# Performance work log

Hardware: AMD Instinct MI355X
Metric: run time of the kernel (lower is better)

## Reference

```python
import jax, jax.numpy as jnp
import numpy as np

NUM_CLUSTERS = 16
CHANNELS = 256
UPDATE_RATE = 0.2
# channels % num_clusters == 0 -> all cluster capacities equal
_BASE = CHANNELS // NUM_CLUSTERS
_REM = CHANNELS % NUM_CLUSTERS
CLUSTER_SIZES = jnp.asarray([_BASE + 1] * _REM + [_BASE] * (NUM_CLUSTERS - _REM), dtype=jnp.int32)


def _cdist(a, b):
    # euclidean pairwise distance, batched over leading dims
    d2 = (jnp.sum(a * a, -1)[..., :, None]
          + jnp.sum(b * b, -1)[..., None, :]
          - 2.0 * (a @ jnp.swapaxes(b, -1, -2)))
    return jnp.sqrt(jnp.clip(d2, 0.0))


def _fps(D, k):
    # farthest point sampling given full [N,N] distance matrix
    start = jnp.argmax(D.sum(1))
    def step(min_d, _):
        far = jnp.argmax(min_d)
        return jnp.minimum(min_d, D[far]), far
    _, rest = jax.lax.scan(step, D[start], None, length=k - 1)
    return jnp.concatenate([start[None], rest])


def _capacity_assign(D, sizes):
    # greedy fixed-capacity assignment, sequential over channels
    order = jnp.argsort(D, axis=1)  # [C, K] cluster preference per channel
    def step(counts, row):
        avail = counts[row] < sizes[row]
        chosen = row[jnp.argmax(avail)]  # first available preference
        return counts.at[chosen].add(1), chosen
    _, assign = jax.lax.scan(step, jnp.zeros(sizes.shape[0], jnp.int32), order)
    return assign


def setup_inputs() -> dict:
    key = jax.random.key(0)
    k1, k2 = jax.random.split(key)
    features = jax.random.normal(k1, (8, CHANNELS, 64, 256), dtype=jnp.float32)
    pos_emb_batch = jax.random.normal(k2, (8, CHANNELS, 3), dtype=jnp.float32)
    return {"features": features, "pos_emb_batch": pos_emb_batch}


def reference(features, pos_emb_batch):
    b, c, nw, df = features.shape
    K = NUM_CLUSTERS
    pos = pos_emb_batch[0]                                   # [C, 3] (module's pos_emb buffer)
    # _initialize_centers: FPS over electrode positions
    centers = pos[_fps(_cdist(pos, pos), K)]                 # [K, 3]
    # _find_farthest_channels (euclidean): FPS over flattened features per batch
    ff = features.reshape(b, c, -1)
    Db = _cdist(ff, ff)                                      # [b, C, C]
    sel = jax.vmap(lambda D: _fps(D, K))(Db)                 # [b, K]
    # _cluster_euclidean_temp: nearest temp center per channel
    center_coords = pos_emb_batch[jnp.arange(b)[:, None], sel]      # [b, K, 3]
    temp_assign = jnp.argmin(_cdist(pos_emb_batch, center_coords), -1)  # [b, C]
    # per-cluster mean of positions over the whole batch
    flat_a = temp_assign.reshape(-1)
    flat_p = pos_emb_batch.reshape(-1, 3)
    sums = jax.ops.segment_sum(flat_p, flat_a, num_segments=K)
    cnts = jax.ops.segment_sum(jnp.ones(flat_a.shape, jnp.float32), flat_a, num_segments=K)
    avg = jnp.where(cnts[:, None] > 0, sums / jnp.maximum(cnts, 1.0)[:, None], 0.0)
    # match old centers to batch-average temp centers and EMA update
    matching = jnp.argmin(_cdist(centers, avg), axis=1)
    centers = (1.0 - UPDATE_RATE) * centers + UPDATE_RATE * avg[matching]
    # capacity-constrained final assignment
    return _capacity_assign(_cdist(pos, centers), CLUSTER_SIZES)
```

## Files before the change

kernel.cpp:

```cpp
#include <hip/hip_runtime.h>

#define NB 8
#define NC 256
#define DF 16384
#define KCL 16
#define SPLITS 16
#define KC (DF / SPLITS)
#define BK 32
#define ITERS (KC / BK)
#define NPAIR 3
#define GEMM_BLOCKS (NPAIR * 2 * NB * SPLITS)

typedef _Float16 half8 __attribute__((ext_vector_type(8)));
typedef _Float16 half4_t __attribute__((ext_vector_type(4)));
typedef float floatx4 __attribute__((ext_vector_type(4)));

__device__ const int TItab[NPAIR] = {0,0,1};
__device__ const int TJtab[NPAIR] = {0,1,1};

__device__ __forceinline__ int argmax256(float v, float* sv, int* si) {
  int t = threadIdx.x;
  sv[t] = v; si[t] = t;
  __syncthreads();
  #pragma unroll
  for (int s = 128; s >= 1; s >>= 1) {
    if (t < s) {
      float a = sv[t], b = sv[t + s];
      int ia = si[t], ib = si[t + s];
      if (b > a || (b == a && ib < ia)) { sv[t] = b; si[t] = ib; }
    }
    __syncthreads();
  }
  int r = si[0];
  __syncthreads();
  return r;
}

__device__ __forceinline__ int argmax512p(float v, float* sv, int* si) {
  int t = threadIdx.x;
  sv[t] = v; si[t] = t;
  __syncthreads();
  #pragma unroll
  for (int s = 256; s >= 1; s >>= 1) {
    if (t < s) {
      float a = sv[t], b = sv[t + s];
      int ia = si[t], ib = si[t + s];
      if (b > a || (b == a && ib < ia)) { sv[t] = b; si[t] = ib; }
    }
    __syncthreads();
  }
  int r = si[0];
  __syncthreads();
  return r;
}

__global__ __launch_bounds__(512, 3) void k_gemm_pre(const float* __restrict__ ff,
                                                     const float* __restrict__ pe,
                                                     float* __restrict__ Pp,
                                                     float* __restrict__ centers0,
                                                     float* __restrict__ rs) {
  __shared__ _Float16 Ah[128][40];
  __shared__ _Float16 Al[128][40];
  __shared__ _Float16 Bh[64][40];
  __shared__ _Float16 Bl[64][40];

  const int bid = blockIdx.x;
  const int tid = threadIdx.x;

  if (bid == GEMM_BLOCKS) {
    float* sm = (float*)&Ah[0][0];
    float* px = sm;        float* py = sm + 256;
    float* pz = sm + 512;  float* pn = sm + 768;
    float* sv = sm + 1024; int*   si = (int*)(sm + 1536);
    int* fpsIdx = (int*)(sm + 2048);
    const int t = tid;
    for (int i = t; i < NB * NC; i += 512) rs[i] = 0.f;
    const bool valid = t < NC;
    float x = 0.f, y = 0.f, z = 0.f, n = 0.f;
    if (valid) {
      x = pe[t * 3 + 0]; y = pe[t * 3 + 1]; z = pe[t * 3 + 2];
      n = x * x + y * y + z * z;
      px[t] = x; py[t] = y; pz[t] = z; pn[t] = n;
    }
    __syncthreads();
    float rsum = -3.4e38f;
    if (valid) {
      rsum = 0.f;
      for (int j = 0; j < NC; ++j) {
        float dot = x * px[j] + y * py[j] + z * pz[j];
        rsum += sqrtf(fmaxf(n + pn[j] - 2.f * dot, 0.f));
      }
    }
    int start = argmax512p(rsum, sv, si);
    if (t == 0) fpsIdx[0] = start;
    float mind = -3.4e38f;
    if (valid) {
      float dot0 = x * px[start] + y * py[start] + z * pz[start];
      mind = sqrtf(fmaxf(n + pn[start] - 2.f * dot0, 0.f));
    }
    for (int it = 1; it < KCL; ++it) {
      int far = argmax512p(mind, sv, si);
      if (t == 0) fpsIdx[it] = far;
      if (valid) {
        float dot = x * px[far] + y * py[far] + z * pz[far];
        mind = fminf(mind, sqrtf(fmaxf(n + pn[far] - 2.f * dot, 0.f)));
      }
    }
    __syncthreads();
    if (t < KCL) {
      int p = fpsIdx[t];
      centers0[t * 3 + 0] = px[p];
      centers0[t * 3 + 1] = py[p];
      centers0[t * 3 + 2] = pz[p];
    }
    return;
  }

  const int x    = bid & 7;
  const int slot = bid >> 3;
  const int tc   = slot % 6;
  const int u    = slot / 6;
  const int gi   = x * 16 + u;
  const int b    = gi & 7;
  const int sp   = gi >> 3;

  const int pair = tc >> 1, ch = tc & 1;
  const int ti = TItab[pair], tj = TJtab[pair];
  const bool diag = (ti == tj);

  const int wave = tid >> 6, lane = tid & 63;
  const int wr = wave >> 1, wc = wave & 1;
  const int lrow = lane & 15, q = lane >> 4;

  const int srA = tid >> 2, scA = (tid & 3) * 8;
  const int srB = tid >> 3, scB = (tid & 7) * 4;
  const float* gA = ff + ((size_t)(b * NC + ti * 128 + srA)) * DF + sp * KC + scA;
  const float* gB = ff + ((size_t)(b * NC + tj * 128 + ch * 64 + srB)) * DF + sp * KC + scB;

  floatx4 a1[2][2], a2[2][2], a3[2][2];
  #pragma unroll
  for (int i = 0; i < 2; ++i)
    #pragma unroll
    for (int j = 0; j < 2; ++j) { a1[i][j] = (floatx4)0.f; a2[i][j] = (floatx4)0.f; a3[i][j] = (floatx4)0.f; }

  float4 ra0 = *(const float4*)(gA), ra1 = *(const float4*)(gA + 4);
  float4 rb = make_float4(0.f, 0.f, 0.f, 0.f);
  if (!diag) rb = *(const float4*)(gB);
  gA += BK; gB += BK;

  for (int it = 0; it < ITERS; ++it) {
    float fa[8] = {ra0.x, ra0.y, ra0.z, ra0.w, ra1.x, ra1.y, ra1.z, ra1.w};
    half8 ah, al;
    #pragma unroll
    for (int e = 0; e < 8; ++e) {
      _Float16 h = (_Float16)fa[e];
      ah[e] = h;
      al[e] = (_Float16)(fa[e] - (float)h);
    }
    half4_t bh4, bl4;
    if (!diag) {
      float fb[4] = {rb.x, rb.y, rb.z, rb.w};
      #pragma unroll
      for (int e = 0; e < 4; ++e) {
        _Float16 h = (_Float16)fb[e];
        bh4[e] = h;
        bl4[e] = (_Float16)(fb[e] - (float)h);
      }
    }
    __syncthreads();
    *(half8*)&Ah[srA][scA] = ah;
    *(half8*)&Al[srA][scA] = al;
    if (!diag) {
      *(half4_t*)&Bh[srB][scB] = bh4;
      *(half4_t*)&Bl[srB][scB] = bl4;
    }
    __syncthreads();
    if (it + 1 < ITERS) {
      ra0 = *(const float4*)(gA); ra1 = *(const float4*)(gA + 4);
      if (!diag) rb = *(const float4*)(gB);
      gA += BK; gB += BK;
    }
    const _Float16* bhp = diag ? &Ah[ch * 64][0] : &Bh[0][0];
    const _Float16* blp = diag ? &Al[ch * 64][0] : &Bl[0][0];
    half8 af[2], lf[2];
    #pragma unroll
    for (int i = 0; i < 2; ++i) {
      af[i] = *(const half8*)&Ah[wr * 32 + i * 16 + lrow][q * 8];
      lf[i] = *(const half8*)&Al[wr * 32 + i * 16 + lrow][q * 8];
    }
    #pragma unroll
    for (int j = 0; j < 2; ++j) {
      half8 bhf = *(const half8*)(bhp + (wc * 32 + j * 16 + lrow) * 40 + q * 8);
      half8 blf = *(const half8*)(blp + (wc * 32 + j * 16 + lrow) * 40 + q * 8);
      #pragma unroll
      for (int i = 0; i < 2; ++i) {
        a1[i][j] = __builtin_amdgcn_mfma_f32_16x16x32_f16(af[i], bhf, a1[i][j], 0, 0, 0);
        a2[i][j] = __builtin_amdgcn_mfma_f32_16x16x32_f16(af[i], blf, a2[i][j], 0, 0, 0);
        a3[i][j] = __builtin_amdgcn_mfma_f32_16x16x32_f16(lf[i], bhf, a3[i][j], 0, 0, 0);
      }
    }
  }

  float* Pb = Pp + (size_t)(sp * NB + b) * NC * NC;
  #pragma unroll
  for (int i = 0; i < 2; ++i) {
    int grow = ti * 128 + wr * 32 + i * 16 + q * 4;
    #pragma unroll
    for (int j = 0; j < 2; ++j) {
      int gcol = tj * 128 + ch * 64 + wc * 32 + j * 16 + lrow;
      float4 v;
      v.x = a1[i][j][0] + a2[i][j][0] + a3[i][j][0];
      v.y = a1[i][j][1] + a2[i][j][1] + a3[i][j][1];
      v.z = a1[i][j][2] + a2[i][j][2] + a3[i][j][2];
      v.w = a1[i][j][3] + a2[i][j][3] + a3[i][j][3];
      Pb[(size_t)(grow + 0) * NC + gcol] = v.x;
      Pb[(size_t)(grow + 1) * NC + gcol] = v.y;
      Pb[(size_t)(grow + 2) * NC + gcol] = v.z;
      Pb[(size_t)(grow + 3) * NC + gcol] = v.w;
      if (!diag) *(float4*)&Pb[(size_t)gcol * NC + grow] = v;
    }
  }
}

__global__ __launch_bounds__(256) void k_formD(const float* __restrict__ Pp,
                                               float* __restrict__ Db,
                                               float* __restrict__ rs) {
  __shared__ float dg_s[NC];
  const int t = threadIdx.x;
  const int b = blockIdx.x >> 5, i0 = (blockIdx.x & 31) * 8;
  float s = 0.f;
  #pragma unroll
  for (int sp = 0; sp < SPLITS; ++sp)
    s += Pp[((size_t)(sp * NB + b) * NC + t) * NC + t];
  dg_s[t] = s;
  __syncthreads();
  float colsum = 0.f;
  for (int ii = 0; ii < 8; ++ii) {
    int i = i0 + ii;
    float acc = 0.f;
    #pragma unroll
    for (int sp = 0; sp < SPLITS; ++sp)
      acc += Pp[((size_t)(sp * NB + b) * NC + i) * NC + t];
    float d2 = dg_s[i] + dg_s[t] - 2.f * acc;
    float d = sqrtf(fmaxf(d2, 0.f));
    Db[((size_t)b * NC + i) * NC + t] = d;
    colsum += d;
  }
  atomicAdd(&rs[b * NC + t], colsum);
}

__global__ __launch_bounds__(256) void k_fps_b(const float* __restrict__ Db,
                                               const float* __restrict__ rs,
                                               const float* __restrict__ pe,
                                               float* __restrict__ ccoord) {
  int b = blockIdx.x, t = threadIdx.x;
  const float* D = Db + (size_t)b * NC * NC;
  __shared__ float sv[NC]; __shared__ int si[NC];
  __shared__ int fpsIdx[KCL];
  int start = argmax256(rs[b * NC + t], sv, si);
  if (t == 0) fpsIdx[0] = start;
  float mind = D[start * NC + t];
  for (int it = 1; it < KCL; ++it) {
    int far = argmax256(mind, sv, si);
    if (t == 0) fpsIdx[it] = far;
    mind = fminf(mind, D[far * NC + t]);
  }
  __syncthreads();
  if (t < KCL) {
    int p = fpsIdx[t];
    ccoord[(b * KCL + t) * 3 + 0] = pe[(b * NC + p) * 3 + 0];
    ccoord[(b * KCL + t) * 3 + 1] = pe[(b * NC + p) * 3 + 1];
    ccoord[(b * KCL + t) * 3 + 2] = pe[(b * NC + p) * 3 + 2];
  }
}

__global__ __launch_bounds__(256) void k_final(const float* __restrict__ pe,
                                               const float* __restrict__ ccoord,
                                               const float* __restrict__ centers0,
                                               int* __restrict__ outp) {
  __shared__ float cc[NB * KCL * 3];
  __shared__ float cn[NB * KCL];
  __shared__ float sums[KCL][3];
  __shared__ int cnts[KCL];
  __shared__ float avg[KCL][3];
  __shared__ float an[KCL];
  __shared__ float c0[KCL * 3];
  __shared__ float c1x[KCL], c1y[KCL], c1z[KCL], c1n[KCL];
  __shared__ int order[NC][KCL];
  int t = threadIdx.x;
  for (int i = t; i < NB * KCL * 3; i += 256) cc[i] = ccoord[i];
  if (t < KCL * 3) c0[t] = centers0[t];
  if (t < KCL) { sums[t][0] = 0.f; sums[t][1] = 0.f; sums[t][2] = 0.f; cnts[t] = 0; }
  __syncthreads();
  if (t < NB * KCL) {
    float x = cc[t * 3], y = cc[t * 3 + 1], z = cc[t * 3 + 2];
    cn[t] = x * x + y * y + z * z;
  }
  __syncthreads();
  for (int b = 0; b < NB; ++b) {
    int p = b * NC + t;
    float x = pe[p * 3], y = pe[p * 3 + 1], z = pe[p * 3 + 2];
    float n = x * x + y * y + z * z;
    float best = 3.4e38f; int bi = 0;
    #pragma unroll
    for (int k = 0; k < KCL; ++k) {
      int c = b * KCL + k;
      float dot = x * cc[c * 3] + y * cc[c * 3 + 1] + z * cc[c * 3 + 2];
      float d2 = fmaxf(n + cn[c] - 2.f * dot, 0.f);
      if (d2 < best) { best = d2; bi = k; }
    }
    atomicAdd(&sums[bi][0], x);
    atomicAdd(&sums[bi][1], y);
    atomicAdd(&sums[bi][2], z);
    atomicAdd(&cnts[bi], 1);
  }
  __syncthreads();
  if (t < KCL) {
    float c = (float)cnts[t];
    float inv = 1.f / fmaxf(c, 1.f);
    float ax = (cnts[t] > 0) ? sums[t][0] * inv : 0.f;
    float ay = (cnts[t] > 0) ? sums[t][1] * inv : 0.f;
    float az = (cnts[t] > 0) ? sums[t][2] * inv : 0.f;
    avg[t][0] = ax; avg[t][1] = ay; avg[t][2] = az;
    an[t] = ax * ax + ay * ay + az * az;
  }
  __syncthreads();
  if (t < KCL) {
    float x = c0[t * 3], y = c0[t * 3 + 1], z = c0[t * 3 + 2];
    float n = x * x + y * y + z * z;
    float best = 3.4e38f; int bi = 0;
    #pragma unroll
    for (int j = 0; j < KCL; ++j) {
      float dot = x * avg[j][0] + y * avg[j][1] + z * avg[j][2];
      float d2 = fmaxf(n + an[j] - 2.f * dot, 0.f);
      if (d2 < best) { best = d2; bi = j; }
    }
    float nx = 0.8f * x + 0.2f * avg[bi][0];
    float ny = 0.8f * y + 0.2f * avg[bi][1];
    float nz = 0.8f * z + 0.2f * avg[bi][2];
    c1x[t] = nx; c1y[t] = ny; c1z[t] = nz;
    c1n[t] = nx * nx + ny * ny + nz * nz;
  }
  __syncthreads();
  {
    float x = pe[t * 3], y = pe[t * 3 + 1], z = pe[t * 3 + 2];
    float n = x * x + y * y + z * z;
    float v[KCL];
    #pragma unroll
    for (int k = 0; k < KCL; ++k) {
      float dot = x * c1x[k] + y * c1y[k] + z * c1z[k];
      v[k] = fmaxf(n + c1n[k] - 2.f * dot, 0.f);
    }
    bool used[KCL];
    #pragma unroll
    for (int k = 0; k < KCL; ++k) used[k] = false;
    for (int r = 0; r < KCL; ++r) {
      float best = 3.4e38f; int bi = 0;
      #pragma unroll
      for (int j = 0; j < KCL; ++j) {
        if (!used[j] && v[j] < best) { best = v[j]; bi = j; }
      }
      order[t][r] = bi;
      used[bi] = true;
    }
  }
  __syncthreads();
  if (t < 64) {
    int cnt = 0;
    int cur = (t < KCL) ? order[0][t] : 0;
    for (int i = 0; i < NC; ++i) {
      int nxt = (t < KCL && i + 1 < NC) ? order[i + 1][t] : 0;
      int ccur = __shfl(cnt, cur);
      bool avail = (t < KCL) && (ccur < 16);
      unsigned long long m = __ballot(avail);
      int chosen;
      if (m != 0ull) {
        int rank = __ffsll((unsigned long long)m) - 1;
        chosen = __shfl(cur, rank);
      } else {
        chosen = __shfl(cur, 0);
      }
      if (t == chosen) cnt++;
      if (t == 0) outp[i] = chosen;
      cur = nxt;
    }
  }
}

extern "C" void kernel_launch(void* const* d_in, const int* in_sizes, int n_in,
                              void* d_out, int out_size, void* d_ws, size_t ws_size,
                              hipStream_t stream) {
  (void)in_sizes; (void)n_in; (void)out_size; (void)ws_size;
  const float* features = (const float*)d_in[0];
  const float* pe = (const float*)d_in[1];
  char* ws = (char*)d_ws;
  float* Pp       = (float*)(ws);
  float* Db       = (float*)(ws + 33554432);
  float* rs       = (float*)(ws + 35651584);
  float* centers0 = (float*)(ws + 35659776);
  float* ccoord   = (float*)(ws + 35660288);
  int*   outp     = (int*)d_out;

  hipLaunchKernelGGL(k_gemm_pre, dim3(GEMM_BLOCKS + 1), dim3(512), 0, stream,
                     features, pe, Pp, centers0, rs);
  hipLaunchKernelGGL(k_formD, dim3(256), dim3(256), 0, stream, Pp, Db, rs);
  hipLaunchKernelGGL(k_fps_b, dim3(NB), dim3(256), 0, stream, Db, rs, pe, ccoord);
  hipLaunchKernelGGL(k_final, dim3(1), dim3(256), 0, stream, pe, ccoord, centers0, outp);
}
```

Measured before the change: 328.9 us.

## Halve GEMM block threads, enlarge per-wave tile, use wave-shuffle argmax

```diff
diff --git a/kernel.cpp b/kernel.cpp
--- a/kernel.cpp
+++ b/kernel.cpp
@@ -18,43 +18,29 @@
 __device__ const int TItab[NPAIR] = {0,0,1};
 __device__ const int TJtab[NPAIR] = {0,1,1};
 
-__device__ __forceinline__ int argmax256(float v, float* sv, int* si) {
+__device__ __forceinline__ int argmax256w(float v, float* sv, int* si) {
   int t = threadIdx.x;
-  sv[t] = v; si[t] = t;
-  __syncthreads();
-  #pragma unroll
-  for (int s = 128; s >= 1; s >>= 1) {
-    if (t < s) {
-      float a = sv[t], b = sv[t + s];
-      int ia = si[t], ib = si[t + s];
-      if (b > a || (b == a && ib < ia)) { sv[t] = b; si[t] = ib; }
-    }
-    __syncthreads();
-  }
-  int r = si[0];
-  __syncthreads();
-  return r;
-}
-
-__device__ __forceinline__ int argmax512p(float v, float* sv, int* si) {
-  int t = threadIdx.x;
-  sv[t] = v; si[t] = t;
-  __syncthreads();
-  #pragma unroll
-  for (int s = 256; s >= 1; s >>= 1) {
-    if (t < s) {
-      float a = sv[t], b = sv[t + s];
-      int ia = si[t], ib = si[t + s];
-      if (b > a || (b == a && ib < ia)) { sv[t] = b; si[t] = ib; }
-    }
-    __syncthreads();
-  }
-  int r = si[0];
-  __syncthreads();
-  return r;
-}
-
-__global__ __launch_bounds__(512, 3) void k_gemm_pre(const float* __restrict__ ff,
+  float bv = v; int bi = t;
+  #pragma unroll
+  for (int s = 32; s >= 1; s >>= 1) {
+    float ov = __shfl_down(bv, s);
+    int   oi = __shfl_down(bi, s);
+    if (ov > bv || (ov == bv && oi < bi)) { bv = ov; bi = oi; }
+  }
+  int w = t >> 6;
+  if ((t & 63) == 0) { sv[w] = bv; si[w] = bi; }
+  __syncthreads();
+  float rbv = sv[0]; int rbi = si[0];
+  #pragma unroll
+  for (int k = 1; k < 4; ++k) {
+    float ov = sv[k]; int oi = si[k];
+    if (ov > rbv || (ov == rbv && oi < rbi)) { rbv = ov; rbi = oi; }
+  }
+  __syncthreads();
+  return rbi;
+}
+
+__global__ __launch_bounds__(256, 3) void k_gemm_pre(const float* __restrict__ ff,
                                                      const float* __restrict__ pe,
                                                      float* __restrict__ Pp,
                                                      float* __restrict__ centers0,
@@ -71,40 +57,28 @@
     float* sm = (float*)&Ah[0][0];
     float* px = sm;        float* py = sm + 256;
     float* pz = sm + 512;  float* pn = sm + 768;
-    float* sv = sm + 1024; int*   si = (int*)(sm + 1536);
-    int* fpsIdx = (int*)(sm + 2048);
+    float* sv = sm + 1024; int*   si = (int*)(sm + 1280);
+    int* fpsIdx = (int*)(sm + 1536);
     const int t = tid;
-    for (int i = t; i < NB * NC; i += 512) rs[i] = 0.f;
-    const bool valid = t < NC;
-    float x = 0.f, y = 0.f, z = 0.f, n = 0.f;
-    if (valid) {
-      x = pe[t * 3 + 0]; y = pe[t * 3 + 1]; z = pe[t * 3 + 2];
-      n = x * x + y * y + z * z;
-      px[t] = x; py[t] = y; pz[t] = z; pn[t] = n;
-    }
+    for (int i = t; i < NB * NC; i += 256) rs[i] = 0.f;
+    float x = pe[t * 3 + 0], y = pe[t * 3 + 1], z = pe[t * 3 + 2];
+    float n = x * x + y * y + z * z;
+    px[t] = x; py[t] = y; pz[t] = z; pn[t] = n;
     __syncthreads();
-    float rsum = -3.4e38f;
-    if (valid) {
-      rsum = 0.f;
-      for (int j = 0; j < NC; ++j) {
-        float dot = x * px[j] + y * py[j] + z * pz[j];
-        rsum += sqrtf(fmaxf(n + pn[j] - 2.f * dot, 0.f));
-      }
-    }
-    int start = argmax512p(rsum, sv, si);
+    float rsum = 0.f;
+    for (int j = 0; j < NC; ++j) {
+      float dot = x * px[j] + y * py[j] + z * pz[j];
+      rsum += sqrtf(fmaxf(n + pn[j] - 2.f * dot, 0.f));
+    }
+    int start = argmax256w(rsum, sv, si);
     if (t == 0) fpsIdx[0] = start;
-    float mind = -3.4e38f;
-    if (valid) {
-      float dot0 = x * px[start] + y * py[start] + z * pz[start];
-      mind = sqrtf(fmaxf(n + pn[start] - 2.f * dot0, 0.f));
-    }
+    float dot0 = x * px[start] + y * py[start] + z * pz[start];
+    float mind = sqrtf(fmaxf(n + pn[start] - 2.f * dot0, 0.f));
     for (int it = 1; it < KCL; ++it) {
-      int far = argmax512p(mind, sv, si);
+      int far = argmax256w(mind, sv, si);
       if (t == 0) fpsIdx[it] = far;
-      if (valid) {
-        float dot = x * px[far] + y * py[far] + z * pz[far];
-        mind = fminf(mind, sqrtf(fmaxf(n + pn[far] - 2.f * dot, 0.f)));
-      }
+      float dot = x * px[far] + y * py[far] + z * pz[far];
+      mind = fminf(mind, sqrtf(fmaxf(n + pn[far] - 2.f * dot, 0.f)));
     }
     __syncthreads();
     if (t < KCL) {
@@ -133,86 +107,101 @@
   const int lrow = lane & 15, q = lane >> 4;
 
   const int srA = tid >> 2, scA = (tid & 3) * 8;
-  const int srB = tid >> 3, scB = (tid & 7) * 4;
-  const float* gA = ff + ((size_t)(b * NC + ti * 128 + srA)) * DF + sp * KC + scA;
-  const float* gB = ff + ((size_t)(b * NC + tj * 128 + ch * 64 + srB)) * DF + sp * KC + scB;
-
-  floatx4 a1[2][2], a2[2][2], a3[2][2];
-  #pragma unroll
-  for (int i = 0; i < 2; ++i)
-    #pragma unroll
-    for (int j = 0; j < 2; ++j) { a1[i][j] = (floatx4)0.f; a2[i][j] = (floatx4)0.f; a3[i][j] = (floatx4)0.f; }
-
-  float4 ra0 = *(const float4*)(gA), ra1 = *(const float4*)(gA + 4);
-  float4 rb = make_float4(0.f, 0.f, 0.f, 0.f);
-  if (!diag) rb = *(const float4*)(gB);
-  gA += BK; gB += BK;
+  const int srB = tid >> 2, scB = (tid & 3) * 8;
+  const float* gA0 = ff + ((size_t)(b * NC + ti * 128 + srA)) * DF + sp * KC + scA;
+  const float* gA1 = gA0 + (size_t)64 * DF;
+  const float* gB  = ff + ((size_t)(b * NC + tj * 128 + ch * 64 + srB)) * DF + sp * KC + scB;
+
+  floatx4 a1[4][2], c23[4][2];
+  #pragma unroll
+  for (int i = 0; i < 4; ++i)
+    #pragma unroll
+    for (int j = 0; j < 2; ++j) { a1[i][j] = (floatx4)0.f; c23[i][j] = (floatx4)0.f; }
+
+  float4 ra0 = *(const float4*)(gA0), ra1 = *(const float4*)(gA0 + 4);
+  float4 ra2 = *(const float4*)(gA1), ra3 = *(const float4*)(gA1 + 4);
+  float4 rb0 = make_float4(0.f, 0.f, 0.f, 0.f), rb1 = rb0;
+  if (!diag) { rb0 = *(const float4*)(gB); rb1 = *(const float4*)(gB + 4); }
+  gA0 += BK; gA1 += BK; gB += BK;
 
   for (int it = 0; it < ITERS; ++it) {
-    float fa[8] = {ra0.x, ra0.y, ra0.z, ra0.w, ra1.x, ra1.y, ra1.z, ra1.w};
-    half8 ah, al;
-    #pragma unroll
-    for (int e = 0; e < 8; ++e) {
-      _Float16 h = (_Float16)fa[e];
-      ah[e] = h;
-      al[e] = (_Float16)(fa[e] - (float)h);
-    }
-    half4_t bh4, bl4;
+    half8 ah0, al0, ah1, al1;
+    half8 bh8 = (half8)(_Float16)0.f, bl8 = (half8)(_Float16)0.f;
+    {
+      float f[8] = {ra0.x, ra0.y, ra0.z, ra0.w, ra1.x, ra1.y, ra1.z, ra1.w};
+      #pragma unroll
+      for (int e = 0; e < 8; ++e) {
+        _Float16 h = (_Float16)f[e];
+        ah0[e] = h; al0[e] = (_Float16)(f[e] - (float)h);
+      }
+    }
+    {
+      float f[8] = {ra2.x, ra2.y, ra2.z, ra2.w, ra3.x, ra3.y, ra3.z, ra3.w};
+      #pragma unroll
+      for (int e = 0; e < 8; ++e) {
+        _Float16 h = (_Float16)f[e];
+        ah1[e] = h; al1[e] = (_Float16)(f[e] - (float)h);
+      }
+    }
     if (!diag) {
-      float fb[4] = {rb.x, rb.y, rb.z, rb.w};
-      #pragma unroll
-      for (int e = 0; e < 4; ++e) {
-        _Float16 h = (_Float16)fb[e];
-        bh4[e] = h;
-        bl4[e] = (_Float16)(fb[e] - (float)h);
+      float f[8] = {rb0.x, rb0.y, rb0.z, rb0.w, rb1.x, rb1.y, rb1.z, rb1.w};
+      #pragma unroll
+      for (int e = 0; e < 8; ++e) {
+        _Float16 h = (_Float16)f[e];
+        bh8[e] = h; bl8[e] = (_Float16)(f[e] - (float)h);
       }
     }
     __syncthreads();
-    *(half8*)&Ah[srA][scA] = ah;
-    *(half8*)&Al[srA][scA] = al;
+    *(half8*)&Ah[srA][scA] = ah0;
+    *(half8*)&Al[srA][scA] = al0;
+    *(half8*)&Ah[srA + 64][scA] = ah1;
+    *(half8*)&Al[srA + 64][scA] = al1;
     if (!diag) {
-      *(half4_t*)&Bh[srB][scB] = bh4;
-      *(half4_t*)&Bl[srB][scB] = bl4;
+      *(half8*)&Bh[srB][scB] = bh8;
+      *(half8*)&Bl[srB][scB] = bl8;
     }
     __syncthreads();
     if (it + 1 < ITERS) {
-      ra0 = *(const float4*)(gA); ra1 = *(const float4*)(gA + 4);
-      if (!diag) rb = *(const float4*)(gB);
-      gA += BK; gB += BK;
+      ra0 = *(const float4*)(gA0); ra1 = *(const float4*)(gA0 + 4);
+      ra2 = *(const float4*)(gA1); ra3 = *(const float4*)(gA1 + 4);
+      if (!diag) { rb0 = *(const float4*)(gB); rb1 = *(const float4*)(gB + 4); }
+      gA0 += BK; gA1 += BK; gB += BK;
     }
     const _Float16* bhp = diag ? &Ah[ch * 64][0] : &Bh[0][0];
     const _Float16* blp = diag ? &Al[ch * 64][0] : &Bl[0][0];
-    half8 af[2], lf[2];
-    #pragma unroll
-    for (int i = 0; i < 2; ++i) {
-      af[i] = *(const half8*)&Ah[wr * 32 + i * 16 + lrow][q * 8];
-      lf[i] = *(const half8*)&Al[wr * 32 + i * 16 + lrow][q * 8];
-    }
+    half8 bhf[2], blf[2];
     #pragma unroll
     for (int j = 0; j < 2; ++j) {
-      half8 bhf = *(const half8*)(bhp + (wc * 32 + j * 16 + lrow) * 40 + q * 8);
-      half8 blf = *(const half8*)(blp + (wc * 32 + j * 16 + lrow) * 40 + q * 8);
-      #pragma unroll
-      for (int i = 0; i < 2; ++i) {
-        a1[i][j] = __builtin_amdgcn_mfma_f32_16x16x32_f16(af[i], bhf, a1[i][j], 0, 0, 0);
-        a2[i][j] = __builtin_amdgcn_mfma_f32_16x16x32_f16(af[i], blf, a2[i][j], 0, 0, 0);
-        a3[i][j] = __builtin_amdgcn_mfma_f32_16x16x32_f16(lf[i], bhf, a3[i][j], 0, 0, 0);
-      }
-    }
+      bhf[j] = *(const half8*)(bhp + (wc * 32 + j * 16 + lrow) * 40 + q * 8);
+      blf[j] = *(const half8*)(blp + (wc * 32 + j * 16 + lrow) * 40 + q * 8);
+    }
+    __builtin_amdgcn_s_setprio(1);
+    #pragma unroll
+    for (int i = 0; i < 4; ++i) {
+      half8 a_h = *(const half8*)&Ah[wr * 64 + i * 16 + lrow][q * 8];
+      half8 a_l = *(const half8*)&Al[wr * 64 + i * 16 + lrow][q * 8];
+      #pragma unroll
+      for (int j = 0; j < 2; ++j) {
+        a1[i][j]  = __builtin_amdgcn_mfma_f32_16x16x32_f16(a_h, bhf[j], a1[i][j], 0, 0, 0);
+        c23[i][j] = __builtin_amdgcn_mfma_f32_16x16x32_f16(a_h, blf[j], c23[i][j], 0, 0, 0);
+        c23[i][j] = __builtin_amdgcn_mfma_f32_16x16x32_f16(a_l, bhf[j], c23[i][j], 0, 0, 0);
+      }
+    }
+    __builtin_amdgcn_s_setprio(0);
   }
 
   float* Pb = Pp + (size_t)(sp * NB + b) * NC * NC;
   #pragma unroll
-  for (int i = 0; i < 2; ++i) {
-    int grow = ti * 128 + wr * 32 + i * 16 + q * 4;
+  for (int i = 0; i < 4; ++i) {
+    int grow = ti * 128 + wr * 64 + i * 16 + q * 4;
     #pragma unroll
     for (int j = 0; j < 2; ++j) {
       int gcol = tj * 128 + ch * 64 + wc * 32 + j * 16 + lrow;
       float4 v;
-      v.x = a1[i][j][0] + a2[i][j][0] + a3[i][j][0];
-      v.y = a1[i][j][1] + a2[i][j][1] + a3[i][j][1];
-      v.z = a1[i][j][2] + a2[i][j][2] + a3[i][j][2];
-      v.w = a1[i][j][3] + a2[i][j][3] + a3[i][j][3];
+      v.x = a1[i][j][0] + c23[i][j][0];
+      v.y = a1[i][j][1] + c23[i][j][1];
+      v.z = a1[i][j][2] + c23[i][j][2];
+      v.w = a1[i][j][3] + c23[i][j][3];
       Pb[(size_t)(grow + 0) * NC + gcol] = v.x;
       Pb[(size_t)(grow + 1) * NC + gcol] = v.y;
       Pb[(size_t)(grow + 2) * NC + gcol] = v.z;
@@ -255,13 +244,13 @@
                                                float* __restrict__ ccoord) {
   int b = blockIdx.x, t = threadIdx.x;
   const float* D = Db + (size_t)b * NC * NC;
-  __shared__ float sv[NC]; __shared__ int si[NC];
+  __shared__ float sv[4]; __shared__ int si[4];
   __shared__ int fpsIdx[KCL];
-  int start = argmax256(rs[b * NC + t], sv, si);
+  int start = argmax256w(rs[b * NC + t], sv, si);
   if (t == 0) fpsIdx[0] = start;
   float mind = D[start * NC + t];
   for (int it = 1; it < KCL; ++it) {
-    int far = argmax256(mind, sv, si);
+    int far = argmax256w(mind, sv, si);
     if (t == 0) fpsIdx[it] = far;
     mind = fminf(mind, D[far * NC + t]);
   }
@@ -401,7 +390,7 @@
   float* ccoord   = (float*)(ws + 35660288);
   int*   outp     = (int*)d_out;
 
-  hipLaunchKernelGGL(k_gemm_pre, dim3(GEMM_BLOCKS + 1), dim3(512), 0, stream,
+  hipLaunchKernelGGL(k_gemm_pre, dim3(GEMM_BLOCKS + 1), dim3(256), 0, stream,
                      features, pe, Pp, centers0, rs);
   hipLaunchKernelGGL(k_formD, dim3(256), dim3(256), 0, stream, Pp, Db, rs);
   hipLaunchKernelGGL(k_fps_b, dim3(NB), dim3(256), 0, stream, Db, rs, pe, ccoord);
```

New measurement: 324.0 us. About the same (-1.5%).

## Fuse tail kernels into one cooperative kernel and use wave-shuffle argmax

Applied to the files above, without the earlier changes.

```diff
diff --git a/kernel.cpp b/kernel.cpp
--- a/kernel.cpp
+++ b/kernel.cpp
@@ -1,4 +1,7 @@
 #include <hip/hip_runtime.h>
+#include <hip/hip_cooperative_groups.h>
+
+namespace cg = cooperative_groups;
 
 #define NB 8
 #define NC 256
@@ -18,22 +21,26 @@
 __device__ const int TItab[NPAIR] = {0,0,1};
 __device__ const int TJtab[NPAIR] = {0,1,1};
 
-__device__ __forceinline__ int argmax256(float v, float* sv, int* si) {
+__device__ __forceinline__ int argmax256w(float v, float* sv, int* si) {
   int t = threadIdx.x;
-  sv[t] = v; si[t] = t;
+  float bv = v; int bi = t;
+  #pragma unroll
+  for (int s = 32; s >= 1; s >>= 1) {
+    float ov = __shfl_down(bv, s);
+    int   oi = __shfl_down(bi, s);
+    if (ov > bv || (ov == bv && oi < bi)) { bv = ov; bi = oi; }
+  }
+  int w = t >> 6;
+  if ((t & 63) == 0) { sv[w] = bv; si[w] = bi; }
   __syncthreads();
+  float rbv = sv[0]; int rbi = si[0];
   #pragma unroll
-  for (int s = 128; s >= 1; s >>= 1) {
-    if (t < s) {
-      float a = sv[t], b = sv[t + s];
-      int ia = si[t], ib = si[t + s];
-      if (b > a || (b == a && ib < ia)) { sv[t] = b; si[t] = ib; }
-    }
-    __syncthreads();
-  }
-  int r = si[0];
+  for (int k = 1; k < 4; ++k) {
+    float ov = sv[k]; int oi = si[k];
+    if (ov > rbv || (ov == rbv && oi < rbi)) { rbv = ov; rbi = oi; }
+  }
   __syncthreads();
-  return r;
+  return rbi;
 }
 
 __device__ __forceinline__ int argmax512p(float v, float* sv, int* si) {
@@ -157,7 +164,7 @@
       ah[e] = h;
       al[e] = (_Float16)(fa[e] - (float)h);
     }
-    half4_t bh4, bl4;
+    half4_t bh4 = (half4_t)(_Float16)0.f, bl4 = (half4_t)(_Float16)0.f;
     if (!diag) {
       float fb[4] = {rb.x, rb.y, rb.z, rb.w};
       #pragma unroll
@@ -222,167 +229,172 @@
   }
 }
 
-__global__ __launch_bounds__(256) void k_formD(const float* __restrict__ Pp,
-                                               float* __restrict__ Db,
-                                               float* __restrict__ rs) {
-  __shared__ float dg_s[NC];
+__global__ __launch_bounds__(256) void k_tail(const float* __restrict__ Pp,
+                                              float* __restrict__ Db,
+                                              float* __restrict__ rs,
+                                              const float* __restrict__ pe,
+                                              float* __restrict__ ccoord,
+                                              const float* __restrict__ centers0,
+                                              int* __restrict__ outp) {
+  cg::grid_group grid = cg::this_grid();
   const int t = threadIdx.x;
-  const int b = blockIdx.x >> 5, i0 = (blockIdx.x & 31) * 8;
-  float s = 0.f;
-  #pragma unroll
-  for (int sp = 0; sp < SPLITS; ++sp)
-    s += Pp[((size_t)(sp * NB + b) * NC + t) * NC + t];
-  dg_s[t] = s;
-  __syncthreads();
-  float colsum = 0.f;
-  for (int ii = 0; ii < 8; ++ii) {
-    int i = i0 + ii;
-    float acc = 0.f;
+
+  {
+    __shared__ float dg_s[NC];
+    const int b = blockIdx.x >> 5, i0 = (blockIdx.x & 31) * 8;
+    float s = 0.f;
     #pragma unroll
     for (int sp = 0; sp < SPLITS; ++sp)
-      acc += Pp[((size_t)(sp * NB + b) * NC + i) * NC + t];
-    float d2 = dg_s[i] + dg_s[t] - 2.f * acc;
-    float d = sqrtf(fmaxf(d2, 0.f));
-    Db[((size_t)b * NC + i) * NC + t] = d;
-    colsum += d;
-  }
-  atomicAdd(&rs[b * NC + t], colsum);
-}
-
-__global__ __launch_bounds__(256) void k_fps_b(const float* __restrict__ Db,
-                                               const float* __restrict__ rs,
-                                               const float* __restrict__ pe,
-                                               float* __restrict__ ccoord) {
-  int b = blockIdx.x, t = threadIdx.x;
-  const float* D = Db + (size_t)b * NC * NC;
-  __shared__ float sv[NC]; __shared__ int si[NC];
-  __shared__ int fpsIdx[KCL];
-  int start = argmax256(rs[b * NC + t], sv, si);
-  if (t == 0) fpsIdx[0] = start;
-  float mind = D[start * NC + t];
-  for (int it = 1; it < KCL; ++it) {
-    int far = argmax256(mind, sv, si);
-    if (t == 0) fpsIdx[it] = far;
-    mind = fminf(mind, D[far * NC + t]);
-  }
-  __syncthreads();
-  if (t < KCL) {
-    int p = fpsIdx[t];
-    ccoord[(b * KCL + t) * 3 + 0] = pe[(b * NC + p) * 3 + 0];
-    ccoord[(b * KCL + t) * 3 + 1] = pe[(b * NC + p) * 3 + 1];
-    ccoord[(b * KCL + t) * 3 + 2] = pe[(b * NC + p) * 3 + 2];
-  }
-}
-
-__global__ __launch_bounds__(256) void k_final(const float* __restrict__ pe,
-                                               const float* __restrict__ ccoord,
-                                               const float* __restrict__ centers0,
-                                               int* __restrict__ outp) {
-  __shared__ float cc[NB * KCL * 3];
-  __shared__ float cn[NB * KCL];
-  __shared__ float sums[KCL][3];
-  __shared__ int cnts[KCL];
-  __shared__ float avg[KCL][3];
-  __shared__ float an[KCL];
-  __shared__ float c0[KCL * 3];
-  __shared__ float c1x[KCL], c1y[KCL], c1z[KCL], c1n[KCL];
-  __shared__ int order[NC][KCL];
-  int t = threadIdx.x;
-  for (int i = t; i < NB * KCL * 3; i += 256) cc[i] = ccoord[i];
-  if (t < KCL * 3) c0[t] = centers0[t];
-  if (t < KCL) { sums[t][0] = 0.f; sums[t][1] = 0.f; sums[t][2] = 0.f; cnts[t] = 0; }
-  __syncthreads();
-  if (t < NB * KCL) {
-    float x = cc[t * 3], y = cc[t * 3 + 1], z = cc[t * 3 + 2];
-    cn[t] = x * x + y * y + z * z;
-  }
-  __syncthreads();
-  for (int b = 0; b < NB; ++b) {
-    int p = b * NC + t;
-    float x = pe[p * 3], y = pe[p * 3 + 1], z = pe[p * 3 + 2];
-    float n = x * x + y * y + z * z;
-    float best = 3.4e38f; int bi = 0;
-    #pragma unroll
-    for (int k = 0; k < KCL; ++k) {
-      int c = b * KCL + k;
-      float dot = x * cc[c * 3] + y * cc[c * 3 + 1] + z * cc[c * 3 + 2];
-      float d2 = fmaxf(n + cn[c] - 2.f * dot, 0.f);
-      if (d2 < best) { best = d2; bi = k; }
-    }
-    atomicAdd(&sums[bi][0], x);
-    atomicAdd(&sums[bi][1], y);
-    atomicAdd(&sums[bi][2], z);
-    atomicAdd(&cnts[bi], 1);
-  }
-  __syncthreads();
-  if (t < KCL) {
-    float c = (float)cnts[t];
-    float inv = 1.f / fmaxf(c, 1.f);
-    float ax = (cnts[t] > 0) ? sums[t][0] * inv : 0.f;
-    float ay = (cnts[t] > 0) ? sums[t][1] * inv : 0.f;
-    float az = (cnts[t] > 0) ? sums[t][2] * inv : 0.f;
-    avg[t][0] = ax; avg[t][1] = ay; avg[t][2] = az;
-    an[t] = ax * ax + ay * ay + az * az;
-  }
-  __syncthreads();
-  if (t < KCL) {
-    float x = c0[t * 3], y = c0[t * 3 + 1], z = c0[t * 3 + 2];
-    float n = x * x + y * y + z * z;
-    float best = 3.4e38f; int bi = 0;
-    #pragma unroll
-    for (int j = 0; j < KCL; ++j) {
-      float dot = x * avg[j][0] + y * avg[j][1] + z * avg[j][2];
-      float d2 = fmaxf(n + an[j] - 2.f * dot, 0.f);
-      if (d2 < best) { best = d2; bi = j; }
-    }
-    float nx = 0.8f * x + 0.2f * avg[bi][0];
-    float ny = 0.8f * y + 0.2f * avg[bi][1];
-    float nz = 0.8f * z + 0.2f * avg[bi][2];
-    c1x[t] = nx; c1y[t] = ny; c1z[t] = nz;
-    c1n[t] = nx * nx + ny * ny + nz * nz;
-  }
-  __syncthreads();
+      s += Pp[((size_t)(sp * NB + b) * NC + t) * NC + t];
+    dg_s[t] = s;
+    __syncthreads();
+    float colsum = 0.f;
+    for (int ii = 0; ii < 8; ++ii) {
+      int i = i0 + ii;
+      float acc = 0.f;
+      #pragma unroll
+      for (int sp = 0; sp < SPLITS; ++sp)
+        acc += Pp[((size_t)(sp * NB + b) * NC + i) * NC + t];
+      float d2 = dg_s[i] + dg_s[t] - 2.f * acc;
+      float d = sqrtf(fmaxf(d2, 0.f));
+      Db[((size_t)b * NC + i) * NC + t] = d;
+      colsum += d;
+    }
+    atomicAdd(&rs[b * NC + t], colsum);
+  }
+  grid.sync();
+
   {
-    float x = pe[t * 3], y = pe[t * 3 + 1], z = pe[t * 3 + 2];
-    float n = x * x + y * y + z * z;
-    float v[KCL];
-    #pragma unroll
-    for (int k = 0; k < KCL; ++k) {
-      float dot = x * c1x[k] + y * c1y[k] + z * c1z[k];
-      v[k] = fmaxf(n + c1n[k] - 2.f * dot, 0.f);
-    }
-    bool used[KCL];
-    #pragma unroll
-    for (int k = 0; k < KCL; ++k) used[k] = false;
-    for (int r = 0; r < KCL; ++r) {
+    __shared__ float sv[4]; __shared__ int si[4];
+    __shared__ int fpsIdx[KCL];
+    if (blockIdx.x < NB) {
+      int b = blockIdx.x;
+      const float* D = Db + (size_t)b * NC * NC;
+      int start = argmax256w(rs[b * NC + t], sv, si);
+      if (t == 0) fpsIdx[0] = start;
+      float mind = D[start * NC + t];
+      for (int it = 1; it < KCL; ++it) {
+        int far = argmax256w(mind, sv, si);
+        if (t == 0) fpsIdx[it] = far;
+        mind = fminf(mind, D[far * NC + t]);
+      }
+      __syncthreads();
+      if (t < KCL) {
+        int p = fpsIdx[t];
+        ccoord[(b * KCL + t) * 3 + 0] = pe[(b * NC + p) * 3 + 0];
+        ccoord[(b * KCL + t) * 3 + 1] = pe[(b * NC + p) * 3 + 1];
+        ccoord[(b * KCL + t) * 3 + 2] = pe[(b * NC + p) * 3 + 2];
+      }
+    }
+  }
+  grid.sync();
+
+  if (blockIdx.x == 0) {
+    __shared__ float cc[NB * KCL * 3];
+    __shared__ float cn[NB * KCL];
+    __shared__ float sums[KCL][3];
+    __shared__ int cnts[KCL];
+    __shared__ float avg[KCL][3];
+    __shared__ float an[KCL];
+    __shared__ float c0[KCL * 3];
+    __shared__ float c1x[KCL], c1y[KCL], c1z[KCL], c1n[KCL];
+    __shared__ int order[NC][KCL];
+    for (int i = t; i < NB * KCL * 3; i += 256) cc[i] = ccoord[i];
+    if (t < KCL * 3) c0[t] = centers0[t];
+    if (t < KCL) { sums[t][0] = 0.f; sums[t][1] = 0.f; sums[t][2] = 0.f; cnts[t] = 0; }
+    __syncthreads();
+    if (t < NB * KCL) {
+      float x = cc[t * 3], y = cc[t * 3 + 1], z = cc[t * 3 + 2];
+      cn[t] = x * x + y * y + z * z;
+    }
+    __syncthreads();
+    for (int b = 0; b < NB; ++b) {
+      int p = b * NC + t;
+      float x = pe[p * 3], y = pe[p * 3 + 1], z = pe[p * 3 + 2];
+      float n = x * x + y * y + z * z;
       float best = 3.4e38f; int bi = 0;
       #pragma unroll
+      for (int k = 0; k < KCL; ++k) {
+        int c = b * KCL + k;
+        float dot = x * cc[c * 3] + y * cc[c * 3 + 1] + z * cc[c * 3 + 2];
+        float d2 = fmaxf(n + cn[c] - 2.f * dot, 0.f);
+        if (d2 < best) { best = d2; bi = k; }
+      }
+      atomicAdd(&sums[bi][0], x);
+      atomicAdd(&sums[bi][1], y);
+      atomicAdd(&sums[bi][2], z);
+      atomicAdd(&cnts[bi], 1);
+    }
+    __syncthreads();
+    if (t < KCL) {
+      float c = (float)cnts[t];
+      float inv = 1.f / fmaxf(c, 1.f);
+      float ax = (cnts[t] > 0) ? sums[t][0] * inv : 0.f;
+      float ay = (cnts[t] > 0) ? sums[t][1] * inv : 0.f;
+      float az = (cnts[t] > 0) ? sums[t][2] * inv : 0.f;
+      avg[t][0] = ax; avg[t][1] = ay; avg[t][2] = az;
+      an[t] = ax * ax + ay * ay + az * az;
+    }
+    __syncthreads();
+    if (t < KCL) {
+      float x = c0[t * 3], y = c0[t * 3 + 1], z = c0[t * 3 + 2];
+      float n = x * x + y * y + z * z;
+      float best = 3.4e38f; int bi = 0;
+      #pragma unroll
       for (int j = 0; j < KCL; ++j) {
-        if (!used[j] && v[j] < best) { best = v[j]; bi = j; }
-      }
-      order[t][r] = bi;
-      used[bi] = true;
-    }
-  }
-  __syncthreads();
-  if (t < 64) {
-    int cnt = 0;
-    int cur = (t < KCL) ? order[0][t] : 0;
-    for (int i = 0; i < NC; ++i) {
-      int nxt = (t < KCL && i + 1 < NC) ? order[i + 1][t] : 0;
-      int ccur = __shfl(cnt, cur);
-      bool avail = (t < KCL) && (ccur < 16);
-      unsigned long long m = __ballot(avail);
-      int chosen;
-      if (m != 0ull) {
-        int rank = __ffsll((unsigned long long)m) - 1;
-        chosen = __shfl(cur, rank);
-      } else {
-        chosen = __shfl(cur, 0);
-      }
-      if (t == chosen) cnt++;
-      if (t == 0) outp[i] = chosen;
-      cur = nxt;
+        float dot = x * avg[j][0] + y * avg[j][1] + z * avg[j][2];
+        float d2 = fmaxf(n + an[j] - 2.f * dot, 0.f);
+        if (d2 < best) { best = d2; bi = j; }
+      }
+      float nx = 0.8f * x + 0.2f * avg[bi][0];
+      float ny = 0.8f * y + 0.2f * avg[bi][1];
+      float nz = 0.8f * z + 0.2f * avg[bi][2];
+      c1x[t] = nx; c1y[t] = ny; c1z[t] = nz;
+      c1n[t] = nx * nx + ny * ny + nz * nz;
+    }
+    __syncthreads();
+    {
+      float x = pe[t * 3], y = pe[t * 3 + 1], z = pe[t * 3 + 2];
+      float n = x * x + y * y + z * z;
+      float v[KCL];
+      #pragma unroll
+      for (int k = 0; k < KCL; ++k) {
+        float dot = x * c1x[k] + y * c1y[k] + z * c1z[k];
+        v[k] = fmaxf(n + c1n[k] - 2.f * dot, 0.f);
+      }
+      bool used[KCL];
+      #pragma unroll
+      for (int k = 0; k < KCL; ++k) used[k] = false;
+      for (int r = 0; r < KCL; ++r) {
+        float best = 3.4e38f; int bi = 0;
+        #pragma unroll
+        for (int j = 0; j < KCL; ++j) {
+          if (!used[j] && v[j] < best) { best = v[j]; bi = j; }
+        }
+        order[t][r] = bi;
+        used[bi] = true;
+      }
+    }
+    __syncthreads();
+    if (t < 64) {
+      int cnt = 0;
+      int cur = (t < KCL) ? order[0][t] : 0;
+      for (int i = 0; i < NC; ++i) {
+        int nxt = (t < KCL && i + 1 < NC) ? order[i + 1][t] : 0;
+        int ccur = __shfl(cnt, cur);
+        bool avail = (t < KCL) && (ccur < 16);
+        unsigned long long m = __ballot(avail);
+        int chosen;
+        if (m != 0ull) {
+          int rank = __ffsll((unsigned long long)m) - 1;
+          chosen = __shfl(cur, rank);
+        } else {
+          chosen = __shfl(cur, 0);
+        }
+        if (t == chosen) cnt++;
+        if (t == 0) outp[i] = chosen;
+        cur = nxt;
+      }
     }
   }
 }
@@ -403,7 +415,8 @@
 
   hipLaunchKernelGGL(k_gemm_pre, dim3(GEMM_BLOCKS + 1), dim3(512), 0, stream,
                      features, pe, Pp, centers0, rs);
-  hipLaunchKernelGGL(k_formD, dim3(256), dim3(256), 0, stream, Pp, Db, rs);
-  hipLaunchKernelGGL(k_fps_b, dim3(NB), dim3(256), 0, stream, Db, rs, pe, ccoord);
-  hipLaunchKernelGGL(k_final, dim3(1), dim3(256), 0, stream, pe, ccoord, centers0, outp);
+
+  void* targs[] = {(void*)&Pp, (void*)&Db, (void*)&rs, (void*)&pe,
+                   (void*)&ccoord, (void*)&centers0, (void*)&outp};
+  hipLaunchCooperativeKernel((void*)k_tail, dim3(256), dim3(256), targs, 0, stream);
 }
```

New measurement: 393.4 us. 1.2x slower.
